# Optimization experiments

Hardware: AMD Instinct MI355X
Metric: run time of the kernel (lower is better)

Reference implementation:

```python
import jax, jax.numpy as jnp
import numpy as np

D = 256
NODE_COUNTS = [200000, 50000, 12000, 4000]  # n_src per block; dst of block l = NODE_COUNTS[l+1]
EDGE_COUNTS = [500000, 120000, 40000]


def setup_inputs() -> dict:
    key = jax.random.key(0)
    ks = jax.random.split(key, 16)
    x = jax.random.normal(ks[0], (NODE_COUNTS[0], D), dtype=jnp.float32)
    inp = {"x": x}
    scale = 1.0 / np.sqrt(D)
    ki = 1
    for l in range(3):
        inp[f"Wself{l}"] = jax.random.normal(ks[ki], (D, D), dtype=jnp.float32) * scale; ki += 1
        inp[f"Wneigh{l}"] = jax.random.normal(ks[ki], (D, D), dtype=jnp.float32) * scale; ki += 1
        inp[f"b{l}"] = jnp.zeros((D,), dtype=jnp.float32)
    for l in range(3):
        e = EDGE_COUNTS[l]
        inp[f"src{l}"] = jax.random.randint(ks[ki], (e,), 0, NODE_COUNTS[l]); ki += 1
        inp[f"dst{l}"] = jax.random.randint(ks[ki], (e,), 0, NODE_COUNTS[l + 1]); ki += 1
    inp["nd0"], inp["nd1"], inp["nd2"] = NODE_COUNTS[1], NODE_COUNTS[2], NODE_COUNTS[3]
    return inp


def _sage_layer(h, src, dst, n_dst, Ws, Wn, b, relu=True):
    # DGL SAGEConv('mean'): out = fc_self(h_dst) + fc_neigh(mean_{u in N(v)} h_u) + bias
    h_dst = h[:n_dst]
    msgs = h[src]                                               # [E, d] gather
    agg = jax.ops.segment_sum(msgs, dst, num_segments=n_dst)    # [n_dst, d]
    deg = jax.ops.segment_sum(jnp.ones((dst.shape[0],), h.dtype), dst, num_segments=n_dst)
    mean = agg / jnp.maximum(deg, 1.0)[:, None]
    out = h_dst @ Ws + mean @ Wn + b
    return jax.nn.relu(out) if relu else out


def reference(x, Wself0, Wneigh0, b0, Wself1, Wneigh1, b1, Wself2, Wneigh2, b2,
              src0, dst0, src1, dst1, src2, dst2, nd0, nd1, nd2):
    h = _sage_layer(x, src0, dst0, nd0, Wself0, Wneigh0, b0)
    h = _sage_layer(h, src1, dst1, nd1, Wself1, Wneigh1, b1)
    h = _sage_layer(h, src2, dst2, nd2, Wself2, Wneigh2, b2)
    return h
```

## Files before the change

### kernel.cpp

```cpp
#include <hip/hip_runtime.h>
#include <stdint.h>

#define D 256

typedef __attribute__((ext_vector_type(8))) short bf16x8;
typedef __attribute__((ext_vector_type(4))) float f32x4;

__device__ inline unsigned short f2bf(float f) {
    union { float f; uint32_t u; } v; v.f = f;
    return (unsigned short)((v.u + 0x7FFFu + ((v.u >> 16) & 1u)) >> 16);
}
__device__ inline float bf2f(unsigned short b) {
    return __uint_as_float(((uint32_t)b) << 16);
}

#define SEG0 0
#define SEG1 50176
#define SEG2 62464
#define CURTOT 66560
#define NBLK 65

#define WBLK 1536
#define XBLK 25000

struct PreArgs {
    const float* w[6];
    const float* x;
    unsigned short* wt;
    unsigned short* xb;
    const int* d0; const int* d1; const int* d2;
    int* cur;
    int E0, E01, Etot, cblk0;
};

__global__ __launch_bounds__(256) void fused_pre(PreArgs a)
{
    int b = blockIdx.x;
    if (b < WBLK) {
        int t = b * 256 + threadIdx.x;
        int m = t >> 16, e = t & 65535;
        int col = e >> 8, k = e & 255;
        a.wt[t] = f2bf(a.w[m][(k << 8) + col]);
    } else if (b < WBLK + XBLK) {
        long t = (long)(b - WBLK) * 256 + threadIdx.x;
        const float4* p = (const float4*)a.x + t * 2;
        float4 v0 = p[0], v1 = p[1];
        unsigned short r[8] = {f2bf(v0.x), f2bf(v0.y), f2bf(v0.z), f2bf(v0.w),
                               f2bf(v1.x), f2bf(v1.y), f2bf(v1.z), f2bf(v1.w)};
        *(uint4*)(a.xb + t * 8) = *(uint4*)r;
    } else {
        int e = (b - a.cblk0) * 256 + threadIdx.x;
        if (e >= a.Etot) return;
        int base, d;
        if (e < a.E0)       { base = SEG0; d = a.d0[e]; }
        else if (e < a.E01) { base = SEG1; d = a.d1[e - a.E0]; }
        else                { base = SEG2; d = a.d2[e - a.E01]; }
        atomicAdd(&a.cur[base + d], 1);
    }
}

__global__ __launch_bounds__(256) void scan_blocks(
    int* __restrict__ cur, int* __restrict__ bsum)
{
    __shared__ int wsum[4];
    int tid = threadIdx.x, lane = tid & 63, wid = tid >> 6;
    int base = blockIdx.x * 1024 + tid * 4;
    int4 v = *(int4*)(cur + base);
    int t0 = v.x, t01 = t0 + v.y, t012 = t01 + v.z, tot = t012 + v.w;
    int incl = tot;
    #pragma unroll
    for (int ofs = 1; ofs < 64; ofs <<= 1) {
        int t = __shfl_up(incl, ofs, 64);
        if (lane >= ofs) incl += t;
    }
    if (lane == 63) wsum[wid] = incl;
    __syncthreads();
    if (tid == 0) {
        int run = 0;
        #pragma unroll
        for (int w = 0; w < 4; ++w) { int t = wsum[w]; wsum[w] = run; run += t; }
        bsum[blockIdx.x] = run;
    }
    __syncthreads();
    int texcl = wsum[wid] + incl - tot;
    v.x = texcl; v.y = texcl + t0; v.z = texcl + t01; v.w = texcl + t012;
    *(int4*)(cur + base) = v;
}

__global__ __launch_bounds__(128) void scan_bsums(
    const int* __restrict__ bsum, int* __restrict__ bscan)
{
    __shared__ int s[NBLK];
    int tid = threadIdx.x;
    if (tid < NBLK) s[tid] = bsum[tid];
    __syncthreads();
    if (tid == 0) {
        int run = 0;
        for (int b = 0; b < 49; ++b)  { int t = s[b]; s[b] = run; run += t; }
        run = 0;
        for (int b = 49; b < 61; ++b) { int t = s[b]; s[b] = run; run += t; }
        run = 0;
        for (int b = 61; b < 65; ++b) { int t = s[b]; s[b] = run; run += t; }
    }
    __syncthreads();
    if (tid < NBLK) bscan[tid] = s[tid];
}

__global__ __launch_bounds__(256) void scan_addback(
    int* __restrict__ cur, const int* __restrict__ bscan)
{
    int base = blockIdx.x * 1024 + threadIdx.x * 4;
    int add = bscan[blockIdx.x];
    int4 v = *(int4*)(cur + base);
    v.x += add; v.y += add; v.z += add; v.w += add;
    *(int4*)(cur + base) = v;
}

__global__ __launch_bounds__(256) void fill_all(
    const int* __restrict__ s0, const int* __restrict__ s1, const int* __restrict__ s2,
    const int* __restrict__ d0, const int* __restrict__ d1, const int* __restrict__ d2,
    int* __restrict__ cur, int* __restrict__ idx, int E0, int E01, int Etot)
{
    int e = blockIdx.x * 256 + threadIdx.x;
    if (e >= Etot) return;
    int base, d, s, ib;
    if (e < E0)       { base = SEG0; d = d0[e];       s = s0[e];       ib = 0; }
    else if (e < E01) { base = SEG1; d = d1[e - E0];  s = s1[e - E0];  ib = E0; }
    else              { base = SEG2; d = d2[e - E01]; s = s2[e - E01]; ib = E01; }
    int p = atomicAdd(&cur[base + d], 1);
    idx[ib + p] = s;
}

__global__ __launch_bounds__(256) void gather_mean_k(
    const unsigned short* __restrict__ h, const int* __restrict__ idx,
    const int* __restrict__ curseg, unsigned short* __restrict__ mean, int M)
{
    int t = blockIdx.x * blockDim.x + threadIdx.x;
    int w = t >> 6, lane = t & 63;
    if (w >= M) return;
    int e0 = w ? curseg[w - 1] : 0;
    int e1 = curseg[w];
    float4 acc = make_float4(0.f, 0.f, 0.f, 0.f);
    int e = e0;
    for (; e + 1 < e1; e += 2) {
        int sa = idx[e], sb = idx[e + 1];
        ushort4 va = *(const ushort4*)(h + (size_t)sa * D + lane * 4);
        ushort4 vb = *(const ushort4*)(h + (size_t)sb * D + lane * 4);
        acc.x += bf2f(va.x) + bf2f(vb.x);
        acc.y += bf2f(va.y) + bf2f(vb.y);
        acc.z += bf2f(va.z) + bf2f(vb.z);
        acc.w += bf2f(va.w) + bf2f(vb.w);
    }
    if (e < e1) {
        int sa = idx[e];
        ushort4 va = *(const ushort4*)(h + (size_t)sa * D + lane * 4);
        acc.x += bf2f(va.x); acc.y += bf2f(va.y);
        acc.z += bf2f(va.z); acc.w += bf2f(va.w);
    }
    float r = 1.0f / fmaxf((float)(e1 - e0), 1.0f);
    ushort4 o;
    o.x = f2bf(acc.x * r); o.y = f2bf(acc.y * r);
    o.z = f2bf(acc.z * r); o.w = f2bf(acc.w * r);
    *(ushort4*)(mean + (size_t)w * D + lane * 4) = o;
}

template<int FINAL>
__global__ __launch_bounds__(256, 2) void sage_gemm_mfma(
    const unsigned short* __restrict__ A1,
    const unsigned short* __restrict__ A2,
    const unsigned short* __restrict__ Wt1,
    const unsigned short* __restrict__ Wt2,
    const float* __restrict__ bias,
    void* __restrict__ outv,
    int M)
{
    __shared__ unsigned short As[128 * 32];
    __shared__ unsigned short Bs[256 * 32];

    int tid = threadIdx.x;
    int lane = tid & 63, wid = tid >> 6;
    int wr = wid >> 1, wc = wid & 1;
    int m0 = blockIdx.x * 128;
    int l15 = lane & 15, lq = lane >> 4;

    f32x4 acc[4][8] = {};

    for (int kt = 0; kt < 16; ++kt) {
        const unsigned short* A = (kt < 8) ? A1 : A2;
        const unsigned short* B = (kt < 8) ? Wt1 : Wt2;
        int kk = (kt & 7) * 32;
        #pragma unroll
        for (int q = 0; q < 2; ++q) {
            int ch = q * 256 + tid;
            int r = ch >> 2, c16 = ch & 3;
            int gr = m0 + r; if (gr >= M) gr = M - 1;
            const unsigned short* src = A + (size_t)gr * 256 + kk + c16 * 8;
            __builtin_amdgcn_global_load_lds(
                (const __attribute__((address_space(1))) void*)src,
                (__attribute__((address_space(3))) void*)(As + (q * 256 + wid * 64) * 8),
                16, 0, 0);
        }
        #pragma unroll
        for (int q = 0; q < 4; ++q) {
            int ch = q * 256 + tid;
            int col = ch >> 2, c16 = ch & 3;
            const unsigned short* src = B + (size_t)col * 256 + kk + c16 * 8;
            __builtin_amdgcn_global_load_lds(
                (const __attribute__((address_space(1))) void*)src,
                (__attribute__((address_space(3))) void*)(Bs + (q * 256 + wid * 64) * 8),
                16, 0, 0);
        }
        __syncthreads();

        bf16x8 af[4], bfr[8];
        #pragma unroll
        for (int i = 0; i < 4; ++i)
            af[i] = *(const bf16x8*)(As + (wr * 64 + i * 16 + l15) * 32 + lq * 8);
        #pragma unroll
        for (int i = 0; i < 8; ++i)
            bfr[i] = *(const bf16x8*)(Bs + (wc * 128 + i * 16 + l15) * 32 + lq * 8);

        #pragma unroll
        for (int mr = 0; mr < 4; ++mr)
            #pragma unroll
            for (int nc = 0; nc < 8; ++nc)
                acc[mr][nc] = __builtin_amdgcn_mfma_f32_16x16x32_bf16(
                    af[mr], bfr[nc], acc[mr][nc], 0, 0, 0);
        __syncthreads();
    }

    #pragma unroll
    for (int nc = 0; nc < 8; ++nc) {
        int gc = wc * 128 + nc * 16 + l15;
        float bv = bias[gc];
        #pragma unroll
        for (int mr = 0; mr < 4; ++mr) {
            #pragma unroll
            for (int reg = 0; reg < 4; ++reg) {
                int gr = m0 + wr * 64 + mr * 16 + lq * 4 + reg;
                if (gr < M) {
                    float v = fmaxf(acc[mr][nc][reg] + bv, 0.f);
                    if (FINAL) ((float*)outv)[(size_t)gr * 256 + gc] = v;
                    else ((unsigned short*)outv)[(size_t)gr * 256 + gc] = f2bf(v);
                }
            }
        }
    }
}

extern "C" void kernel_launch(void* const* d_in, const int* in_sizes, int n_in,
                              void* d_out, int out_size, void* d_ws, size_t ws_size,
                              hipStream_t stream) {
    const float* x = (const float*)d_in[0];
    const float* Wself[3]  = {(const float*)d_in[1], (const float*)d_in[4], (const float*)d_in[7]};
    const float* Wneigh[3] = {(const float*)d_in[2], (const float*)d_in[5], (const float*)d_in[8]};
    const float* bias[3]   = {(const float*)d_in[3], (const float*)d_in[6], (const float*)d_in[9]};
    const int* src[3] = {(const int*)d_in[10], (const int*)d_in[12], (const int*)d_in[14]};
    const int* dst[3] = {(const int*)d_in[11], (const int*)d_in[13], (const int*)d_in[15]};
    int E[3]    = {in_sizes[10], in_sizes[12], in_sizes[14]};
    int ndst[3] = {50000, 12000, 4000};
    int E0 = E[0], E01 = E[0] + E[1], Etot = E[0] + E[1] + E[2];

    unsigned short* xb    = (unsigned short*)d_ws;
    unsigned short* h1b   = xb + (size_t)200000 * D;
    unsigned short* h2b   = h1b + (size_t)50000 * D;
    unsigned short* meanb = h2b + (size_t)12000 * D;
    unsigned short* wt    = meanb + (size_t)50000 * D;
    int* cur   = (int*)(wt + 6 * 65536);
    int* bsum  = cur + CURTOT;
    int* bscan = bsum + 80;
    int* idxa  = bscan + 80;

    hipMemsetAsync(cur, 0, CURTOT * sizeof(int), stream);

    PreArgs pa;
    pa.w[0] = Wself[0]; pa.w[1] = Wneigh[0];
    pa.w[2] = Wself[1]; pa.w[3] = Wneigh[1];
    pa.w[4] = Wself[2]; pa.w[5] = Wneigh[2];
    pa.x = x; pa.wt = wt; pa.xb = xb;
    pa.d0 = dst[0]; pa.d1 = dst[1]; pa.d2 = dst[2];
    pa.cur = cur; pa.E0 = E0; pa.E01 = E01; pa.Etot = Etot;
    pa.cblk0 = WBLK + XBLK;
    int cblk = (Etot + 255) / 256;
    fused_pre<<<WBLK + XBLK + cblk, 256, 0, stream>>>(pa);

    scan_blocks<<<NBLK, 256, 0, stream>>>(cur, bsum);
    scan_bsums<<<1, 128, 0, stream>>>(bsum, bscan);
    scan_addback<<<NBLK, 256, 0, stream>>>(cur, bscan);
    fill_all<<<(Etot + 255) / 256, 256, 0, stream>>>(src[0], src[1], src[2],
        dst[0], dst[1], dst[2], cur, idxa, E0, E01, Etot);

    const unsigned short* hin_b[3] = {xb, h1b, h2b};
    void* houts[3] = {h1b, h2b, d_out};
    int segb[3] = {SEG0, SEG1, SEG2};
    int idxb[3] = {0, E0, E01};

    for (int l = 0; l < 3; ++l) {
        int M = ndst[l];
        int gt = M * 64;
        gather_mean_k<<<(gt + 255) / 256, 256, 0, stream>>>(
            hin_b[l], idxa + idxb[l], cur + segb[l], meanb, M);

        dim3 grid((M + 127) / 128);
        if (l < 2)
            sage_gemm_mfma<0><<<grid, 256, 0, stream>>>(hin_b[l], meanb,
                wt + (size_t)(2 * l) * 65536, wt + (size_t)(2 * l + 1) * 65536,
                bias[l], houts[l], M);
        else
            sage_gemm_mfma<1><<<grid, 256, 0, stream>>>(hin_b[l], meanb,
                wt + (size_t)(2 * l) * 65536, wt + (size_t)(2 * l + 1) * 65536,
                bias[l], houts[l], M);
    }
}
```

Before: 308.2 us.

## Convert only dst rows of x to bf16 and gather layer-0 neighbors from fp32

Shrinks the x-to-bf16 conversion from all 200000 rows to the first 50000 (the rows layer 0's self GEMM reads), and has the layer-0 mean gather read fp32 x directly. This drops the write of a large bf16 copy of x that was only needed for gathers. The trade-off is that each gathered row in layer 0 now reads twice as many bytes. The gather loop is also unrolled to four edges per iteration with two accumulators for more memory-level parallelism.

```diff
diff --git a/kernel.cpp b/kernel.cpp
--- a/kernel.cpp
+++ b/kernel.cpp
@@ -21,7 +21,7 @@
 #define NBLK 65
 
 #define WBLK 1536
-#define XBLK 25000
+#define XBLK 6250
 
 struct PreArgs {
     const float* w[6];
@@ -131,8 +131,9 @@
     idx[ib + p] = s;
 }
 
+template<int BF16IN>
 __global__ __launch_bounds__(256) void gather_mean_k(
-    const unsigned short* __restrict__ h, const int* __restrict__ idx,
+    const void* __restrict__ hv, const int* __restrict__ idx,
     const int* __restrict__ curseg, unsigned short* __restrict__ mean, int M)
 {
     int t = blockIdx.x * blockDim.x + threadIdx.x;
@@ -140,27 +141,56 @@
     if (w >= M) return;
     int e0 = w ? curseg[w - 1] : 0;
     int e1 = curseg[w];
-    float4 acc = make_float4(0.f, 0.f, 0.f, 0.f);
+    float4 acc0 = make_float4(0.f, 0.f, 0.f, 0.f);
+    float4 acc1 = make_float4(0.f, 0.f, 0.f, 0.f);
     int e = e0;
-    for (; e + 1 < e1; e += 2) {
-        int sa = idx[e], sb = idx[e + 1];
-        ushort4 va = *(const ushort4*)(h + (size_t)sa * D + lane * 4);
-        ushort4 vb = *(const ushort4*)(h + (size_t)sb * D + lane * 4);
-        acc.x += bf2f(va.x) + bf2f(vb.x);
-        acc.y += bf2f(va.y) + bf2f(vb.y);
-        acc.z += bf2f(va.z) + bf2f(vb.z);
-        acc.w += bf2f(va.w) + bf2f(vb.w);
-    }
-    if (e < e1) {
-        int sa = idx[e];
-        ushort4 va = *(const ushort4*)(h + (size_t)sa * D + lane * 4);
-        acc.x += bf2f(va.x); acc.y += bf2f(va.y);
-        acc.z += bf2f(va.z); acc.w += bf2f(va.w);
-    }
+    if (BF16IN) {
+        const unsigned short* h = (const unsigned short*)hv;
+        for (; e + 3 < e1; e += 4) {
+            int sa = idx[e], sb = idx[e + 1], sc = idx[e + 2], sd = idx[e + 3];
+            ushort4 va = *(const ushort4*)(h + (size_t)sa * D + lane * 4);
+            ushort4 vb = *(const ushort4*)(h + (size_t)sb * D + lane * 4);
+            ushort4 vc = *(const ushort4*)(h + (size_t)sc * D + lane * 4);
+            ushort4 vd = *(const ushort4*)(h + (size_t)sd * D + lane * 4);
+            acc0.x += bf2f(va.x) + bf2f(vb.x);
+            acc0.y += bf2f(va.y) + bf2f(vb.y);
+            acc0.z += bf2f(va.z) + bf2f(vb.z);
+            acc0.w += bf2f(va.w) + bf2f(vb.w);
+            acc1.x += bf2f(vc.x) + bf2f(vd.x);
+            acc1.y += bf2f(vc.y) + bf2f(vd.y);
+            acc1.z += bf2f(vc.z) + bf2f(vd.z);
+            acc1.w += bf2f(vc.w) + bf2f(vd.w);
+        }
+        for (; e < e1; ++e) {
+            int sa = idx[e];
+            ushort4 va = *(const ushort4*)(h + (size_t)sa * D + lane * 4);
+            acc0.x += bf2f(va.x); acc0.y += bf2f(va.y);
+            acc0.z += bf2f(va.z); acc0.w += bf2f(va.w);
+        }
+    } else {
+        const float* h = (const float*)hv;
+        for (; e + 3 < e1; e += 4) {
+            int sa = idx[e], sb = idx[e + 1], sc = idx[e + 2], sd = idx[e + 3];
+            float4 va = *((const float4*)(h + (size_t)sa * D) + lane);
+            float4 vb = *((const float4*)(h + (size_t)sb * D) + lane);
+            float4 vc = *((const float4*)(h + (size_t)sc * D) + lane);
+            float4 vd = *((const float4*)(h + (size_t)sd * D) + lane);
+            acc0.x += va.x + vb.x; acc0.y += va.y + vb.y;
+            acc0.z += va.z + vb.z; acc0.w += va.w + vb.w;
+            acc1.x += vc.x + vd.x; acc1.y += vc.y + vd.y;
+            acc1.z += vc.z + vd.z; acc1.w += vc.w + vd.w;
+        }
+        for (; e < e1; ++e) {
+            int sa = idx[e];
+            float4 va = *((const float4*)(h + (size_t)sa * D) + lane);
+            acc0.x += va.x; acc0.y += va.y; acc0.z += va.z; acc0.w += va.w;
+        }
+    }
+    acc0.x += acc1.x; acc0.y += acc1.y; acc0.z += acc1.z; acc0.w += acc1.w;
     float r = 1.0f / fmaxf((float)(e1 - e0), 1.0f);
     ushort4 o;
-    o.x = f2bf(acc.x * r); o.y = f2bf(acc.y * r);
-    o.z = f2bf(acc.z * r); o.w = f2bf(acc.w * r);
+    o.x = f2bf(acc0.x * r); o.y = f2bf(acc0.y * r);
+    o.z = f2bf(acc0.z * r); o.w = f2bf(acc0.w * r);
     *(ushort4*)(mean + (size_t)w * D + lane * 4) = o;
 }
 
@@ -262,7 +292,7 @@
     int E0 = E[0], E01 = E[0] + E[1], Etot = E[0] + E[1] + E[2];
 
     unsigned short* xb    = (unsigned short*)d_ws;
-    unsigned short* h1b   = xb + (size_t)200000 * D;
+    unsigned short* h1b   = xb + (size_t)50000 * D;
     unsigned short* h2b   = h1b + (size_t)50000 * D;
     unsigned short* meanb = h2b + (size_t)12000 * D;
     unsigned short* wt    = meanb + (size_t)50000 * D;
@@ -298,8 +328,12 @@
     for (int l = 0; l < 3; ++l) {
         int M = ndst[l];
         int gt = M * 64;
-        gather_mean_k<<<(gt + 255) / 256, 256, 0, stream>>>(
-            hin_b[l], idxa + idxb[l], cur + segb[l], meanb, M);
+        if (l == 0)
+            gather_mean_k<0><<<(gt + 255) / 256, 256, 0, stream>>>(
+                x, idxa + idxb[l], cur + segb[l], meanb, M);
+        else
+            gather_mean_k<1><<<(gt + 255) / 256, 256, 0, stream>>>(
+                hin_b[l], idxa + idxb[l], cur + segb[l], meanb, M);
 
         dim3 grid((M + 127) / 128);
         if (l < 2)
```

Result: faster. 290.2 us (-5.8%).
